# Performance work log

Hardware: AMD Instinct MI355X
Metric: run time of the kernel (lower is better)

## Reference

```python
import jax, jax.numpy as jnp
import numpy as np

EMA_A = 0.4      # exponential moving average decay used in Hash_ExpMovAverage
WIN = 9          # window_size
LN_EPS = 1e-3    # keras LayerNormalization default epsilon


def setup_inputs() -> dict:
    key = jax.random.key(0)
    ks = jax.random.split(key, 8)
    B, N, D, H = 8, 4096, 256, 8
    w = lambda k, shape: jax.random.normal(k, shape, jnp.float32) * 0.05
    return {
        "x": jax.random.normal(ks[0], (B, N, D), jnp.float32),
        "head_kernel": w(ks[1], (D, H, D)),
        "head_bias": w(ks[2], (H, D)),
        "down_kernel": w(ks[3], (H, D, D)),
        "down_bias": w(ks[4], (D,)),
        "value_kernel": w(ks[5], (D, D)),
        "value_bias": w(ks[6], (D,)),
        "ln_gamma": jnp.ones((D,), jnp.float32),
        "ln_beta": jnp.zeros((D,), jnp.float32),
    }


def reference(x, head_kernel, head_bias, down_kernel, down_bias,
              value_kernel, value_bias, ln_gamma, ln_beta):
    B, N, D = x.shape
    half = (WIN - 1) // 2

    # Up_Projection: [B,N,D] -> [B,N,H,D], relu
    q = jax.nn.relu(jnp.einsum('bnd,dhe->bnhe', x, head_kernel) + head_bias)

    # ---- Neighborhoods_Arrangement ----
    # Neighborhood_SimHash: sign codes from relu activations, summed over heads
    codes = 2.0 * jnp.minimum(jnp.ceil(q), 1.0) - 1.0        # [B,N,H,D]
    lsh = jnp.sum(codes, axis=-2)                            # [B,N,D]
    # Hash_ExpMovAverage: sort descending along D, add positional encoding, EMA dot
    pos = jnp.argsort(-lsh, axis=-1)                         # descending order
    lsh_sorted = jnp.take_along_axis(lsh, pos, axis=-1)
    pf = pos.astype(jnp.float32)
    freq = 10.0 ** (-(pf / jnp.float32(D)))                  # 1 / 10**powers
    pe = jnp.sin(freq) * (pf % 2) + jnp.cos(freq) * (1.0 - pf % 2)
    vals = lsh_sorted + pe / EMA_A
    c = EMA_A * (1.0 - EMA_A) ** jnp.arange(D, dtype=jnp.float32)
    simv = jnp.einsum('bnd,d->bn', vals, c)                  # [B,N]
    order = jnp.argsort(simv, axis=-1)                       # ascending
    q = jnp.take_along_axis(q, order[:, :, None, None], axis=1)  # reorder tokens

    # Down_Projection: [B,N,H,D] -> [B,N,D], relu
    q = jax.nn.relu(jnp.einsum('bnhd,hde->bne', q, down_kernel) + down_bias)

    # (matches tile-first / extract_patches / tile-last concat in the original)
    starts = jnp.clip(jnp.arange(N) - half, 0, N - WIN)      # [N]
    widx = starts[:, None] + jnp.arange(WIN)[None, :]
    keyw = q[:, widx]

    scale = jnp.sqrt(jnp.float32(D))
    scores = jax.nn.softmax(jnp.einsum('bnd,bnwd->bnw', q, keyw) / scale, axis=-1)
    value = jax.nn.relu(jnp.einsum('bnwd,de->bnwe', keyw, value_kernel) + value_bias)
    attn_out = jnp.einsum('bnwd,bnw->bnd', value, scores)

    # Residual with ORIGINAL (un-permuted) inputs + LayerNorm (keras default eps)
    y = attn_out + x
    mu = jnp.mean(y, axis=-1, keepdims=True)
    var = jnp.var(y, axis=-1, keepdims=True)
    return (y - mu) / jnp.sqrt(var + LN_EPS) * ln_gamma + ln_beta
```

## Files before the change

kernel.cpp:

```cpp
#include <hip/hip_runtime.h>

constexpr int Bc = 8, Nc = 4096;

using short8 = __attribute__((ext_vector_type(8))) short;
using f32x4  = __attribute__((ext_vector_type(4))) float;

static __device__ __forceinline__ unsigned short f2bf(float f) {
    unsigned u = __float_as_uint(f);
    u += 0x7fffu + ((u >> 16) & 1u);
    return (unsigned short)(u >> 16);
}
static __device__ __forceinline__ int swz(int r, int k) {
    return (r << 9) + ((k << 1) ^ ((r & 7) << 4));
}

__global__ __launch_bounds__(256)
void k0_wdt(const float* __restrict__ Wd, unsigned short* __restrict__ WdT)
{
    __shared__ float tile[64][65];
    const int h  = blockIdx.x >> 4;
    const int t  = blockIdx.x & 15;
    const int kb = (t >> 2) * 64, eb = (t & 3) * 64;
    const int tid = threadIdx.x;
    {
        const int krow = tid >> 2, ec = (tid & 3) * 16;
        const float* src = Wd + h * 65536 + (kb + krow) * 256 + eb + ec;
        #pragma unroll
        for (int i = 0; i < 4; ++i) {
            float4 v = *reinterpret_cast<const float4*>(src + i * 4);
            tile[krow][ec + i * 4 + 0] = v.x;
            tile[krow][ec + i * 4 + 1] = v.y;
            tile[krow][ec + i * 4 + 2] = v.z;
            tile[krow][ec + i * 4 + 3] = v.w;
        }
    }
    __syncthreads();
    {
        const int erow = tid >> 2, dc = (tid & 3) * 16;
        unsigned short o[16];
        #pragma unroll
        for (int i = 0; i < 16; ++i) o[i] = f2bf(tile[dc + i][erow]);
        unsigned short* dst = WdT + h * 65536 + (eb + erow) * 256 + kb + dc;
        *reinterpret_cast<short8*>(dst)     = *reinterpret_cast<short8*>(&o[0]);
        *reinterpret_cast<short8*>(dst + 8) = *reinterpret_cast<short8*>(&o[8]);
    }
}

__global__ __launch_bounds__(256)
void k0_wht(const float* __restrict__ Wh, unsigned short* __restrict__ WhH,
            float* __restrict__ WhT)
{
    __shared__ float tile[64][65];
    const int h  = blockIdx.x >> 4;
    const int t  = blockIdx.x & 15;
    const int kb = (t >> 2) * 64, eb = (t & 3) * 64;
    const int tid = threadIdx.x;
    {
        const int krow = tid >> 2, ec = (tid & 3) * 16;
        const float* src = Wh + (kb + krow) * 2048 + h * 256 + eb + ec;
        #pragma unroll
        for (int i = 0; i < 4; ++i) {
            float4 v = *reinterpret_cast<const float4*>(src + i * 4);
            tile[krow][ec + i * 4 + 0] = v.x;
            tile[krow][ec + i * 4 + 1] = v.y;
            tile[krow][ec + i * 4 + 2] = v.z;
            tile[krow][ec + i * 4 + 3] = v.w;
        }
    }
    __syncthreads();
    {
        const int erow = tid >> 2, dc = (tid & 3) * 16;
        unsigned short o[16];
        float of[16];
        #pragma unroll
        for (int i = 0; i < 16; ++i) {
            of[i] = tile[dc + i][erow];
            o[i] = f2bf(of[i]);
        }
        const long base = (long)h * 65536 + (eb + erow) * 256 + kb + dc;
        *reinterpret_cast<short8*>(WhH + base)     = *reinterpret_cast<short8*>(&o[0]);
        *reinterpret_cast<short8*>(WhH + base + 8) = *reinterpret_cast<short8*>(&o[8]);
        #pragma unroll
        for (int i = 0; i < 16; i += 4)
            *reinterpret_cast<float4*>(WhT + base + i) = *reinterpret_cast<const float4*>(&of[i]);
    }
}

__global__ __launch_bounds__(256)
void k0_wvt(const float* __restrict__ Wv, unsigned short* __restrict__ WvT)
{
    __shared__ float tile[64][65];
    const int t  = blockIdx.x;
    const int kb = (t >> 2) * 64, eb = (t & 3) * 64;
    const int tid = threadIdx.x;
    {
        const int krow = tid >> 2, ec = (tid & 3) * 16;
        const float* src = Wv + (kb + krow) * 256 + eb + ec;
        #pragma unroll
        for (int i = 0; i < 4; ++i) {
            float4 v = *reinterpret_cast<const float4*>(src + i * 4);
            tile[krow][ec + i * 4 + 0] = v.x;
            tile[krow][ec + i * 4 + 1] = v.y;
            tile[krow][ec + i * 4 + 2] = v.z;
            tile[krow][ec + i * 4 + 3] = v.w;
        }
    }
    __syncthreads();
    {
        const int erow = tid >> 2, dc = (tid & 3) * 16;
        unsigned short o[16];
        #pragma unroll
        for (int i = 0; i < 16; ++i) o[i] = f2bf(tile[dc + i][erow]);
        unsigned short* dst = WvT + (eb + erow) * 256 + kb + dc;
        *reinterpret_cast<short8*>(dst)     = *reinterpret_cast<short8*>(&o[0]);
        *reinterpret_cast<short8*>(dst + 8) = *reinterpret_cast<short8*>(&o[8]);
    }
}

#define XSH_OFF  0
#define QTB_OFF  16384
#define VALQ_OFF 35072
#define PE_OFF   67840
#define CF_OFF   68864
#define CNT_OFF  69888
#define FCN_OFF  71936
#define FLS_OFF  71952
#define FLS_CAP  1536
#define GUARD    0.012f

__global__ __launch_bounds__(256, 2)
void k1_head_down(const float* __restrict__ x,
                  const float* __restrict__ bh,
                  const float* __restrict__ WhT,
                  const unsigned short* __restrict__ WhH,
                  const unsigned short* __restrict__ WdT, const float* __restrict__ bd,
                  float* __restrict__ z, float* __restrict__ simv)
{
    __shared__ __align__(16) char SM[78336];

    const int tid = threadIdx.x;
    const long rowbase = (long)blockIdx.x * 32;
    const int wavei = tid >> 6, lane = tid & 63;
    const int mrow = lane & 15, kgrp = lane >> 4;
    const int ebase = wavei * 64 + mrow;
    const int kfo = kgrp * 8;

    short8 hB[4][4], dB[4][4];
    #pragma unroll
    for (int i = 0; i < 4; ++i)
        #pragma unroll
        for (int nf = 0; nf < 4; ++nf)
            hB[i][nf] = *reinterpret_cast<const short8*>(
                &WhH[(ebase + nf * 16) * 256 + i * 32 + kfo]);

    {
        const int d = tid;
        const float u = -((float)d * 0.00390625f);
        const float freq = (float)pow(10.0, (double)u);
        const float pe = (d & 1) ? (float)sin((double)freq)
                                 : (float)cos((double)freq);
        ((float*)(SM + PE_OFF))[d] = __fdiv_rn(pe, 0.4f);
        ((float*)(SM + CF_OFF))[d] = __fmul_rn(0.4f, (float)pow((double)0.6f, (double)d));
    }
    if (tid == 0) *((int*)(SM + FCN_OFF)) = 0;
    {
        const int r = tid >> 3, kc = (tid & 7) * 32;
        const float* src = x + (rowbase + r) * 256 + kc;
        unsigned short oh[32];
        #pragma unroll
        for (int i = 0; i < 32; i += 4) {
            float4 v = *reinterpret_cast<const float4*>(src + i);
            oh[i + 0] = f2bf(v.x); oh[i + 1] = f2bf(v.y);
            oh[i + 2] = f2bf(v.z); oh[i + 3] = f2bf(v.w);
        }
        #pragma unroll
        for (int i = 0; i < 32; i += 8)
            *reinterpret_cast<short8*>(SM + XSH_OFF + swz(r, kc + i)) =
                *reinterpret_cast<short8*>(&oh[i]);
    }

    unsigned lshp[4] = {0u, 0u, 0u, 0u};
    f32x4 dacc[2][4];
    #pragma unroll
    for (int mt = 0; mt < 2; ++mt)
        #pragma unroll
        for (int nf = 0; nf < 4; ++nf) dacc[mt][nf] = (f32x4){0.f, 0.f, 0.f, 0.f};

    __syncthreads();

    for (int h = 0; h < 8; ++h) {
        const unsigned short* whh = WhH + ((long)h << 16);
        const unsigned short* wdh = WdT + ((long)h << 16);
        float bias[4];
        #pragma unroll
        for (int nf = 0; nf < 4; ++nf) bias[nf] = bh[(h << 8) + ebase + nf * 16];

        f32x4 hacc[2][4];
        #pragma unroll
        for (int mt = 0; mt < 2; ++mt)
            #pragma unroll
            for (int nf = 0; nf < 4; ++nf) hacc[mt][nf] = (f32x4){0.f, 0.f, 0.f, 0.f};
        #pragma unroll
        for (int kt = 0; kt < 8; ++kt) {
            const int k0 = kt * 32 + kfo;
            short8 a0 = *reinterpret_cast<const short8*>(SM + XSH_OFF + swz(mrow, k0));
            short8 a1 = *reinterpret_cast<const short8*>(SM + XSH_OFF + swz(16 + mrow, k0));
            if (kt < 4) {
                #pragma unroll
                for (int nf = 0; nf < 4; ++nf)
                    dB[kt][nf] = *reinterpret_cast<const short8*>(
                        &wdh[(ebase + nf * 16) * 256 + kt * 32 + kfo]);
            }
            #pragma unroll
            for (int nf = 0; nf < 4; ++nf) {
                hacc[0][nf] = __builtin_amdgcn_mfma_f32_16x16x32_bf16(a0, hB[kt & 3][nf], hacc[0][nf], 0, 0, 0);
                hacc[1][nf] = __builtin_amdgcn_mfma_f32_16x16x32_bf16(a1, hB[kt & 3][nf], hacc[1][nf], 0, 0, 0);
            }
            if (kt < 4) {
                #pragma unroll
                for (int nf = 0; nf < 4; ++nf)
                    hB[kt][nf] = *reinterpret_cast<const short8*>(
                        &whh[(ebase + nf * 16) * 256 + (kt + 4) * 32 + kfo]);
            }
        }
        #pragma unroll
        for (int mt = 0; mt < 2; ++mt) {
            #pragma unroll
            for (int nf = 0; nf < 4; ++nf) {
                const int e = ebase + nf * 16;
                #pragma unroll
                for (int reg = 0; reg < 4; ++reg) {
                    const int r = mt * 16 + kgrp * 4 + reg;
                    const float pre = __fadd_rn(hacc[mt][nf][reg], bias[nf]);
                    const unsigned pos = (pre > 0.0f) ? 1u : 0u;
                    const int j = mt * 16 + nf * 4 + reg;
                    lshp[j >> 3] += pos << (4 * (j & 7));
                    if (fabsf(pre) < GUARD) {
                        int idx = atomicAdd((int*)(SM + FCN_OFF), 1);
                        if (idx < FLS_CAP)
                            ((int*)(SM + FLS_OFF))[idx] =
                                r | (e << 5) | (h << 13) | ((int)pos << 16);
                    }
                    *reinterpret_cast<unsigned short*>(SM + QTB_OFF + swz(r, e)) =
                        f2bf(fmaxf(pre, 0.0f));
                }
            }
        }
        __syncthreads();
        #pragma unroll
        for (int ks = 0; ks < 8; ++ks) {
            const int k0 = ks * 32 + kfo;
            short8 a0 = *reinterpret_cast<const short8*>(SM + QTB_OFF + swz(mrow, k0));
            short8 a1 = *reinterpret_cast<const short8*>(SM + QTB_OFF + swz(16 + mrow, k0));
            #pragma unroll
            for (int nf = 0; nf < 4; ++nf) {
                dacc[0][nf] = __builtin_amdgcn_mfma_f32_16x16x32_bf16(a0, dB[ks & 3][nf], dacc[0][nf], 0, 0, 0);
                dacc[1][nf] = __builtin_amdgcn_mfma_f32_16x16x32_bf16(a1, dB[ks & 3][nf], dacc[1][nf], 0, 0, 0);
            }
            if (ks < 4) {
                #pragma unroll
                for (int nf = 0; nf < 4; ++nf)
                    dB[ks][nf] = *reinterpret_cast<const short8*>(
                        &wdh[(ebase + nf * 16) * 256 + (ks + 4) * 32 + kfo]);
            } else if (h < 7) {
                #pragma unroll
                for (int nf = 0; nf < 4; ++nf)
                    hB[ks - 4][nf] = *reinterpret_cast<const short8*>(
                        &WhH[((long)(h + 1) << 16) + (ebase + nf * 16) * 256 + (ks - 4) * 32 + kfo]);
            }
        }
        __syncthreads();
    }
    #pragma unroll
    for (int mt = 0; mt < 2; ++mt) {
        #pragma unroll
        for (int nf = 0; nf < 4; ++nf) {
            const int e = ebase + nf * 16;
            const float b = bd[e];
            #pragma unroll
            for (int reg = 0; reg < 4; ++reg)
                z[(rowbase + mt * 16 + kgrp * 4 + reg) * 256 + e] =
                    fmaxf(dacc[mt][nf][reg] + b, 0.0f);
        }
    }
    {
        int* lshI = (int*)SM;
        #pragma unroll
        for (int mt = 0; mt < 2; ++mt)
            #pragma unroll
            for (int nf = 0; nf < 4; ++nf) {
                const int e = ebase + nf * 16;
                #pragma unroll
                for (int reg = 0; reg < 4; ++reg) {
                    const int r = mt * 16 + kgrp * 4 + reg;
                    const int j = mt * 16 + nf * 4 + reg;
                    const unsigned p = (lshp[j >> 3] >> (4 * (j & 7))) & 15u;
                    lshI[e * 34 + r] = 2 * (int)p - 8;
                }
            }
    }
    __syncthreads();
    {
        int* lshI = (int*)SM;
        int n = *((int*)(SM + FCN_OFF));
        n = n < FLS_CAP ? n : FLS_CAP;
        for (int i = tid; i < n; i += 256) {
            const int ent = ((int*)(SM + FLS_OFF))[i];
            const int r = ent & 31, e = (ent >> 5) & 255, hh2 = (ent >> 13) & 7;
            const int fs = ((ent >> 16) & 1) ? 1 : -1;
            const float* xr = x + (rowbase + r) * 256;
            const float* wrow = WhT + (((long)hh2 << 8) + e) * 256;
            float acc = 0.0f;
            for (int k = 0; k < 256; k += 4) {
                float4 xv = *reinterpret_cast<const float4*>(xr + k);
                float4 wv = *reinterpret_cast<const float4*>(wrow + k);
                acc = fmaf(xv.x, wv.x, acc);
                acc = fmaf(xv.y, wv.y, acc);
                acc = fmaf(xv.z, wv.z, acc);
                acc = fmaf(xv.w, wv.w, acc);
            }
            const float pre = __fadd_rn(acc, bh[hh2 * 256 + e]);
            const int es = (pre > 0.0f) ? 1 : -1;
            if (es != fs)
                atomicAdd(&lshI[e * 34 + r], es - fs);
        }
    }
    __syncthreads();
    if (tid < 32) {
        const int r = tid;
        const int* lshI = (const int*)SM;
        const float* pe_over = (const float*)(SM + PE_OFF);
        const float* c_f = (const float*)(SM + CF_OFF);
        int* cw = (int*)(SM + CNT_OFF) + r * 16;
        for (int i = 0; i < 9; ++i) cw[i] = 0;
        for (int d = 0; d < 256; ++d) {
            int vv = lshI[d * 34 + r];
            cw[(vv + 8) >> 1] += 1;
        }
        int run = 0;
        for (int bin = 8; bin >= 0; --bin) { int c0 = cw[bin]; cw[bin] = run; run += c0; }
        float* valq = (float*)(SM + VALQ_OFF + r * 1024);
        for (int d = 0; d < 256; ++d) {
            int vv = lshI[d * 34 + r];
            int bin = (vv + 8) >> 1;
            int j = cw[bin]++;
            valq[j] = __fadd_rn((float)vv, pe_over[d]);
        }
        float L0 = 0.f, L1 = 0.f, L2 = 0.f, L3 = 0.f,
              L4 = 0.f, L5 = 0.f, L6 = 0.f, L7 = 0.f;
        for (int i = 0; i < 256; i += 8) {
            L0 = fmaf(valq[i + 0], c_f[i + 0], L0);
            L1 = fmaf(valq[i + 1], c_f[i + 1], L1);
            L2 = fmaf(valq[i + 2], c_f[i + 2], L2);
            L3 = fmaf(valq[i + 3], c_f[i + 3], L3);
            L4 = fmaf(valq[i + 4], c_f[i + 4], L4);
            L5 = fmaf(valq[i + 5], c_f[i + 5], L5);
            L6 = fmaf(valq[i + 6], c_f[i + 6], L6);
            L7 = fmaf(valq[i + 7], c_f[i + 7], L7);
        }
        const float h0 = __fadd_rn(L0, L4);
        const float h1 = __fadd_rn(L1, L5);
        const float h2 = __fadd_rn(L2, L6);
        const float h3 = __fadd_rn(L3, L7);
        simv[rowbase + r] = __fadd_rn(__fadd_rn(h0, h2), __fadd_rn(h1, h3));
    }
}

__global__ __launch_bounds__(256)
void k2_rank(const float* __restrict__ simv, int* __restrict__ order)
{
    __shared__ float s_l[4096];
    const int b = blockIdx.x >> 4;
    const int chunk = blockIdx.x & 15;
    const float* S = simv + (long)b * 4096;
    for (int i = threadIdx.x; i < 4096; i += 256) s_l[i] = S[i];
    __syncthreads();
    const int n = chunk * 256 + threadIdx.x;
    const float key = s_l[n];
    int cnt = 0;
    for (int m = 0; m < 4096; ++m) {
        float sm = s_l[m];
        cnt += (sm < key) ? 1 : ((sm == key && m < n) ? 1 : 0);
    }
    order[(long)b * 4096 + cnt] = n;
}

__global__ __launch_bounds__(256, 3)
void k3_value(const float* __restrict__ z, const int* __restrict__ order,
              const unsigned short* __restrict__ WvT, const float* __restrict__ bv,
              float* __restrict__ v)
{
    __shared__ __align__(16) unsigned short ZB[32 * 256];
    __shared__ int ord[32];
    const int tid = threadIdx.x;
    const long rowbase = (long)blockIdx.x * 32;
    const long bbase = (rowbase >> 12) << 12;
    const int wavei = tid >> 6, lane = tid & 63;
    const int mrow = lane & 15, kgrp = lane >> 4;
    const int ebase = wavei * 64 + mrow;
    const int kfo = kgrp * 8;

    if (tid < 32) ord[tid] = order[rowbase + tid];

    short8 vB[4][4];
    #pragma unroll
    for (int i = 0; i < 4; ++i)
        #pragma unroll
        for (int nf = 0; nf < 4; ++nf)
            vB[i][nf] = *reinterpret_cast<const short8*>(
                &WvT[(ebase + nf * 16) * 256 + i * 32 + kfo]);

    __syncthreads();
    {
        const int r = tid >> 3, kc = (tid & 7) * 32;
        const float* src = z + (bbase + ord[r]) * 256 + kc;
        unsigned short oh[32];
        #pragma unroll
        for (int i = 0; i < 32; i += 4) {
            float4 vv = *reinterpret_cast<const float4*>(src + i);
            oh[i + 0] = f2bf(vv.x); oh[i + 1] = f2bf(vv.y);
            oh[i + 2] = f2bf(vv.z); oh[i + 3] = f2bf(vv.w);
        }
        #pragma unroll
        for (int i = 0; i < 32; i += 8)
            *reinterpret_cast<short8*>((char*)ZB + swz(r, kc + i)) =
                *reinterpret_cast<short8*>(&oh[i]);
    }
    __syncthreads();

    f32x4 acc[2][4];
    #pragma unroll
    for (int mt = 0; mt < 2; ++mt)
        #pragma unroll
        for (int nf = 0; nf < 4; ++nf) acc[mt][nf] = (f32x4){0.f, 0.f, 0.f, 0.f};
    #pragma unroll
    for (int kt = 0; kt < 8; ++kt) {
        const int k0 = kt * 32 + kfo;
        short8 a0 = *reinterpret_cast<const short8*>((char*)ZB + swz(mrow, k0));
        short8 a1 = *reinterpret_cast<const short8*>((char*)ZB + swz(16 + mrow, k0));
        #pragma unroll
        for (int nf = 0; nf < 4; ++nf) {
            acc[0][nf] = __builtin_amdgcn_mfma_f32_16x16x32_bf16(a0, vB[kt & 3][nf], acc[0][nf], 0, 0, 0);
            acc[1][nf] = __builtin_amdgcn_mfma_f32_16x16x32_bf16(a1, vB[kt & 3][nf], acc[1][nf], 0, 0, 0);
        }
        if (kt < 4) {
            #pragma unroll
            for (int nf = 0; nf < 4; ++nf)
                vB[kt][nf] = *reinterpret_cast<const short8*>(
                    &WvT[(ebase + nf * 16) * 256 + (kt + 4) * 32 + kfo]);
        }
    }
    #pragma unroll
    for (int mt = 0; mt < 2; ++mt) {
        #pragma unroll
        for (int nf = 0; nf < 4; ++nf) {
            const int e = ebase + nf * 16;
            const float b = bv[e];
            #pragma unroll
            for (int reg = 0; reg < 4; ++reg)
                v[(rowbase + mt * 16 + kgrp * 4 + reg) * 256 + e] =
                    fmaxf(acc[mt][nf][reg] + b, 0.0f);
        }
    }
}

__global__ __launch_bounds__(256)
void k4_attn_ln(const float* __restrict__ z, const float* __restrict__ v,
                const int* __restrict__ order, const float* __restrict__ x,
                const float* __restrict__ gamma, const float* __restrict__ beta,
                float* __restrict__ out)
{
    const int tid = threadIdx.x;
    const int wv = tid >> 6, lane = tid & 63;
    const long row = (long)blockIdx.x * 4 + wv;
    const int n = (int)(row & 4095);
    const long bbase = row - n;
    int start = n - 4;
    start = start < 0 ? 0 : start;
    start = start > (Nc - 9) ? (Nc - 9) : start;
    const int d0 = lane * 4;

    const int srcq = order[bbase + n];
    float4 q4 = *reinterpret_cast<const float4*>(&z[(bbase + srcq) * 256 + d0]);

    float t[9];
    #pragma unroll
    for (int w = 0; w < 9; ++w) {
        int srcm = order[bbase + start + w];
        float4 kv = *reinterpret_cast<const float4*>(&z[(bbase + srcm) * 256 + d0]);
        float p = q4.x * kv.x + q4.y * kv.y + q4.z * kv.z + q4.w * kv.w;
        #pragma unroll
        for (int off = 32; off > 0; off >>= 1) p += __shfl_xor(p, off);
        t[w] = p * 0.0625f;
    }
    float mx = t[0];
    #pragma unroll
    for (int w = 1; w < 9; ++w) mx = fmaxf(mx, t[w]);
    float pw[9], psum = 0.0f;
    #pragma unroll
    for (int w = 0; w < 9; ++w) { pw[w] = expf(t[w] - mx); psum += pw[w]; }
    const float pinv = 1.0f / psum;

    float4 a = make_float4(0.f, 0.f, 0.f, 0.f);
    #pragma unroll
    for (int w = 0; w < 9; ++w) {
        float4 vv = *reinterpret_cast<const float4*>(&v[(bbase + start + w) * 256 + d0]);
        float s = pw[w] * pinv;
        a.x = fmaf(vv.x, s, a.x);
        a.y = fmaf(vv.y, s, a.y);
        a.z = fmaf(vv.z, s, a.z);
        a.w = fmaf(vv.w, s, a.w);
    }
    float4 xv = *reinterpret_cast<const float4*>(&x[(bbase + n) * 256 + d0]);
    float4 y = make_float4(a.x + xv.x, a.y + xv.y, a.z + xv.z, a.w + xv.w);

    float s1 = y.x + y.y + y.z + y.w;
    float s2 = y.x * y.x + y.y * y.y + y.z * y.z + y.w * y.w;
    #pragma unroll
    for (int off = 32; off > 0; off >>= 1) {
        s1 += __shfl_xor(s1, off);
        s2 += __shfl_xor(s2, off);
    }
    const float mu = s1 * (1.0f / 256.0f);
    const float var = s2 * (1.0f / 256.0f) - mu * mu;
    const float istd = 1.0f / sqrtf(var + 0.001f);

    float4 g4 = *reinterpret_cast<const float4*>(&gamma[d0]);
    float4 b4 = *reinterpret_cast<const float4*>(&beta[d0]);
    float4 o;
    o.x = (y.x - mu) * istd * g4.x + b4.x;
    o.y = (y.y - mu) * istd * g4.y + b4.y;
    o.z = (y.z - mu) * istd * g4.z + b4.z;
    o.w = (y.w - mu) * istd * g4.w + b4.w;
    *reinterpret_cast<float4*>(&out[row * 256 + d0]) = o;
}

extern "C" void kernel_launch(void* const* d_in, const int* in_sizes, int n_in,
                              void* d_out, int out_size, void* d_ws, size_t ws_size,
                              hipStream_t stream)
{
    const float* x  = (const float*)d_in[0];
    const float* Wh = (const float*)d_in[1];
    const float* bh = (const float*)d_in[2];
    const float* Wd = (const float*)d_in[3];
    const float* bd = (const float*)d_in[4];
    const float* Wv = (const float*)d_in[5];
    const float* bv = (const float*)d_in[6];
    const float* g  = (const float*)d_in[7];
    const float* be = (const float*)d_in[8];
    float* out = (float*)d_out;

    char* ws = (char*)d_ws;
    float*          z     = (float*)ws;
    float*          v     = (float*)(ws + 33554432);
    float*          simv  = (float*)(ws + 67108864);
    int*            order = (int*)(ws + 67239936);
    unsigned short* WdT   = (unsigned short*)(ws + 67371008);
    unsigned short* WhH   = (unsigned short*)(ws + 68419584);
    float*          WhT   = (float*)(ws + 69468160);
    unsigned short* WvT   = (unsigned short*)(ws + 71565312);

    const int rows = Bc * Nc;
    k0_wdt<<<dim3(128), dim3(256), 0, stream>>>(Wd, WdT);
    k0_wht<<<dim3(128), dim3(256), 0, stream>>>(Wh, WhH, WhT);
    k0_wvt<<<dim3(16), dim3(256), 0, stream>>>(Wv, WvT);
    k1_head_down<<<dim3(rows / 32), dim3(256), 0, stream>>>(x, bh, WhT, WhH, WdT, bd, z, simv);
    k2_rank<<<dim3(Bc * 16), dim3(256), 0, stream>>>(simv, order);
    k3_value<<<dim3(rows / 32), dim3(256), 0, stream>>>(z, order, WvT, bv, v);
    k4_attn_ln<<<dim3(rows / 4), dim3(256), 0, stream>>>(z, v, order, x, g, be, out);
}
```

Baseline: 744.2 us.

## Shrink k1 shared memory and weight register buffers to raise occupancy

Compacts k1's LDS layout. The lsh counts become int8, the valq scratch reuses the front of shared memory, and the fallback list shrinks, so the block fits in under 50 KB and the launch bound rises from 2 to 3 blocks per CU. The 4-slot weight register ring in k1 and k3 becomes a 3-slot ring prefetched two k-steps ahead, which lowers VGPR pressure but leaves less latency slack per load. The lsh correction atomics are replaced by a bounded list that one thread applies serially, and x loads and z stores use nontemporal hints. Risks are overflow of the smaller caps (1024 and 96 entries) and more exposed global-load latency.

```diff
diff --git a/kernel.cpp b/kernel.cpp
--- a/kernel.cpp
+++ b/kernel.cpp
@@ -119,16 +119,19 @@
 
 #define XSH_OFF  0
 #define QTB_OFF  16384
-#define VALQ_OFF 35072
-#define PE_OFF   67840
-#define CF_OFF   68864
-#define CNT_OFF  69888
-#define FCN_OFF  71936
-#define FLS_OFF  71952
-#define FLS_CAP  1536
+#define LSH8_OFF 32768
+#define PE_OFF   40960
+#define CF_OFF   41984
+#define CNT_OFF  43008
+#define FCN_OFF  45056
+#define CCN_OFF  45060
+#define FLS_OFF  45064
+#define CLS_OFF  49160
+#define FLS_CAP  1024
+#define CLS_CAP  96
 #define GUARD    0.012f
 
-__global__ __launch_bounds__(256, 2)
+__global__ __launch_bounds__(256, 3)
 void k1_head_down(const float* __restrict__ x,
                   const float* __restrict__ bh,
                   const float* __restrict__ WhT,
@@ -136,7 +139,7 @@
                   const unsigned short* __restrict__ WdT, const float* __restrict__ bd,
                   float* __restrict__ z, float* __restrict__ simv)
 {
-    __shared__ __align__(16) char SM[78336];
+    __shared__ __align__(16) char SM[49600];
 
     const int tid = threadIdx.x;
     const long rowbase = (long)blockIdx.x * 32;
@@ -145,9 +148,9 @@
     const int ebase = wavei * 64 + mrow;
     const int kfo = kgrp * 8;
 
-    short8 hB[4][4], dB[4][4];
-    #pragma unroll
-    for (int i = 0; i < 4; ++i)
+    short8 hB[3][4], dB[3][4];
+    #pragma unroll
+    for (int i = 0; i < 2; ++i)
         #pragma unroll
         for (int nf = 0; nf < 4; ++nf)
             hB[i][nf] = *reinterpret_cast<const short8*>(
@@ -162,16 +165,16 @@
         ((float*)(SM + PE_OFF))[d] = __fdiv_rn(pe, 0.4f);
         ((float*)(SM + CF_OFF))[d] = __fmul_rn(0.4f, (float)pow((double)0.6f, (double)d));
     }
-    if (tid == 0) *((int*)(SM + FCN_OFF)) = 0;
+    if (tid == 0) { *((int*)(SM + FCN_OFF)) = 0; *((int*)(SM + CCN_OFF)) = 0; }
     {
         const int r = tid >> 3, kc = (tid & 7) * 32;
         const float* src = x + (rowbase + r) * 256 + kc;
         unsigned short oh[32];
         #pragma unroll
         for (int i = 0; i < 32; i += 4) {
-            float4 v = *reinterpret_cast<const float4*>(src + i);
-            oh[i + 0] = f2bf(v.x); oh[i + 1] = f2bf(v.y);
-            oh[i + 2] = f2bf(v.z); oh[i + 3] = f2bf(v.w);
+            f32x4 v = __builtin_nontemporal_load(reinterpret_cast<const f32x4*>(src + i));
+            oh[i + 0] = f2bf(v[0]); oh[i + 1] = f2bf(v[1]);
+            oh[i + 2] = f2bf(v[2]); oh[i + 3] = f2bf(v[3]);
         }
         #pragma unroll
         for (int i = 0; i < 32; i += 8)
@@ -205,24 +208,25 @@
             const int k0 = kt * 32 + kfo;
             short8 a0 = *reinterpret_cast<const short8*>(SM + XSH_OFF + swz(mrow, k0));
             short8 a1 = *reinterpret_cast<const short8*>(SM + XSH_OFF + swz(16 + mrow, k0));
-            if (kt < 4) {
+            if (kt < 6) {
                 #pragma unroll
                 for (int nf = 0; nf < 4; ++nf)
-                    dB[kt][nf] = *reinterpret_cast<const short8*>(
-                        &wdh[(ebase + nf * 16) * 256 + kt * 32 + kfo]);
+                    hB[(kt + 2) % 3][nf] = *reinterpret_cast<const short8*>(
+                        &whh[(ebase + nf * 16) * 256 + (kt + 2) * 32 + kfo]);
             }
             #pragma unroll
             for (int nf = 0; nf < 4; ++nf) {
-                hacc[0][nf] = __builtin_amdgcn_mfma_f32_16x16x32_bf16(a0, hB[kt & 3][nf], hacc[0][nf], 0, 0, 0);
-                hacc[1][nf] = __builtin_amdgcn_mfma_f32_16x16x32_bf16(a1, hB[kt & 3][nf], hacc[1][nf], 0, 0, 0);
-            }
-            if (kt < 4) {
-                #pragma unroll
-                for (int nf = 0; nf < 4; ++nf)
-                    hB[kt][nf] = *reinterpret_cast<const short8*>(
-                        &whh[(ebase + nf * 16) * 256 + (kt + 4) * 32 + kfo]);
-            }
-        }
+                hacc[0][nf] = __builtin_amdgcn_mfma_f32_16x16x32_bf16(a0, hB[kt % 3][nf], hacc[0][nf], 0, 0, 0);
+                hacc[1][nf] = __builtin_amdgcn_mfma_f32_16x16x32_bf16(a1, hB[kt % 3][nf], hacc[1][nf], 0, 0, 0);
+            }
+        }
+        #pragma unroll
+        for (int i = 0; i < 2; ++i)
+            #pragma unroll
+            for (int nf = 0; nf < 4; ++nf)
+                dB[i][nf] = *reinterpret_cast<const short8*>(
+                    &wdh[(ebase + nf * 16) * 256 + i * 32 + kfo]);
+
         #pragma unroll
         for (int mt = 0; mt < 2; ++mt) {
             #pragma unroll
@@ -252,21 +256,22 @@
             const int k0 = ks * 32 + kfo;
             short8 a0 = *reinterpret_cast<const short8*>(SM + QTB_OFF + swz(mrow, k0));
             short8 a1 = *reinterpret_cast<const short8*>(SM + QTB_OFF + swz(16 + mrow, k0));
-            #pragma unroll
-            for (int nf = 0; nf < 4; ++nf) {
-                dacc[0][nf] = __builtin_amdgcn_mfma_f32_16x16x32_bf16(a0, dB[ks & 3][nf], dacc[0][nf], 0, 0, 0);
-                dacc[1][nf] = __builtin_amdgcn_mfma_f32_16x16x32_bf16(a1, dB[ks & 3][nf], dacc[1][nf], 0, 0, 0);
-            }
-            if (ks < 4) {
+            if (ks < 6) {
                 #pragma unroll
                 for (int nf = 0; nf < 4; ++nf)
-                    dB[ks][nf] = *reinterpret_cast<const short8*>(
-                        &wdh[(ebase + nf * 16) * 256 + (ks + 4) * 32 + kfo]);
+                    dB[(ks + 2) % 3][nf] = *reinterpret_cast<const short8*>(
+                        &wdh[(ebase + nf * 16) * 256 + (ks + 2) * 32 + kfo]);
             } else if (h < 7) {
+                const int i = ks - 6;
                 #pragma unroll
                 for (int nf = 0; nf < 4; ++nf)
-                    hB[ks - 4][nf] = *reinterpret_cast<const short8*>(
-                        &WhH[((long)(h + 1) << 16) + (ebase + nf * 16) * 256 + (ks - 4) * 32 + kfo]);
+                    hB[i][nf] = *reinterpret_cast<const short8*>(
+                        &WhH[((long)(h + 1) << 16) + (ebase + nf * 16) * 256 + i * 32 + kfo]);
+            }
+            #pragma unroll
+            for (int nf = 0; nf < 4; ++nf) {
+                dacc[0][nf] = __builtin_amdgcn_mfma_f32_16x16x32_bf16(a0, dB[ks % 3][nf], dacc[0][nf], 0, 0, 0);
+                dacc[1][nf] = __builtin_amdgcn_mfma_f32_16x16x32_bf16(a1, dB[ks % 3][nf], dacc[1][nf], 0, 0, 0);
             }
         }
         __syncthreads();
@@ -279,12 +284,13 @@
             const float b = bd[e];
             #pragma unroll
             for (int reg = 0; reg < 4; ++reg)
-                z[(rowbase + mt * 16 + kgrp * 4 + reg) * 256 + e] =
-                    fmaxf(dacc[mt][nf][reg] + b, 0.0f);
-        }
-    }
-    {
-        int* lshI = (int*)SM;
+                __builtin_nontemporal_store(
+                    fmaxf(dacc[mt][nf][reg] + b, 0.0f),
+                    &z[(rowbase + mt * 16 + kgrp * 4 + reg) * 256 + e]);
+        }
+    }
+    {
+        signed char* lsh8 = (signed char*)(SM + LSH8_OFF);
         #pragma unroll
         for (int mt = 0; mt < 2; ++mt)
             #pragma unroll
@@ -295,13 +301,12 @@
                     const int r = mt * 16 + kgrp * 4 + reg;
                     const int j = mt * 16 + nf * 4 + reg;
                     const unsigned p = (lshp[j >> 3] >> (4 * (j & 7))) & 15u;
-                    lshI[e * 34 + r] = 2 * (int)p - 8;
+                    lsh8[e * 32 + r] = (signed char)(2 * (int)p - 8);
                 }
             }
     }
     __syncthreads();
     {
-        int* lshI = (int*)SM;
         int n = *((int*)(SM + FCN_OFF));
         n = n < FLS_CAP ? n : FLS_CAP;
         for (int i = tid; i < n; i += 256) {
@@ -321,27 +326,42 @@
             }
             const float pre = __fadd_rn(acc, bh[hh2 * 256 + e]);
             const int es = (pre > 0.0f) ? 1 : -1;
-            if (es != fs)
-                atomicAdd(&lshI[e * 34 + r], es - fs);
+            if (es != fs) {
+                int ci = atomicAdd((int*)(SM + CCN_OFF), 1);
+                if (ci < CLS_CAP)
+                    ((int*)(SM + CLS_OFF))[ci] = r | (e << 5) | ((es > 0 ? 1 : 0) << 13);
+            }
+        }
+    }
+    __syncthreads();
+    if (tid == 0) {
+        signed char* lsh8 = (signed char*)(SM + LSH8_OFF);
+        int cn = *((int*)(SM + CCN_OFF));
+        cn = cn < CLS_CAP ? cn : CLS_CAP;
+        for (int i = 0; i < cn; ++i) {
+            const int ent = ((int*)(SM + CLS_OFF))[i];
+            const int r = ent & 31, e = (ent >> 5) & 255;
+            const int d = ((ent >> 13) & 1) ? 2 : -2;
+            lsh8[e * 32 + r] = (signed char)(lsh8[e * 32 + r] + d);
         }
     }
     __syncthreads();
     if (tid < 32) {
         const int r = tid;
-        const int* lshI = (const int*)SM;
+        const signed char* lsh8 = (const signed char*)(SM + LSH8_OFF);
         const float* pe_over = (const float*)(SM + PE_OFF);
         const float* c_f = (const float*)(SM + CF_OFF);
         int* cw = (int*)(SM + CNT_OFF) + r * 16;
         for (int i = 0; i < 9; ++i) cw[i] = 0;
         for (int d = 0; d < 256; ++d) {
-            int vv = lshI[d * 34 + r];
+            int vv = (int)lsh8[d * 32 + r];
             cw[(vv + 8) >> 1] += 1;
         }
         int run = 0;
         for (int bin = 8; bin >= 0; --bin) { int c0 = cw[bin]; cw[bin] = run; run += c0; }
-        float* valq = (float*)(SM + VALQ_OFF + r * 1024);
+        float* valq = (float*)(SM + r * 1024);
         for (int d = 0; d < 256; ++d) {
-            int vv = lshI[d * 34 + r];
+            int vv = (int)lsh8[d * 32 + r];
             int bin = (vv + 8) >> 1;
             int j = cw[bin]++;
             valq[j] = __fadd_rn((float)vv, pe_over[d]);
@@ -402,9 +422,9 @@
 
     if (tid < 32) ord[tid] = order[rowbase + tid];
 
-    short8 vB[4][4];
-    #pragma unroll
-    for (int i = 0; i < 4; ++i)
+    short8 vB[3][4];
+    #pragma unroll
+    for (int i = 0; i < 2; ++i)
         #pragma unroll
         for (int nf = 0; nf < 4; ++nf)
             vB[i][nf] = *reinterpret_cast<const short8*>(
@@ -438,16 +458,16 @@
         const int k0 = kt * 32 + kfo;
         short8 a0 = *reinterpret_cast<const short8*>((char*)ZB + swz(mrow, k0));
         short8 a1 = *reinterpret_cast<const short8*>((char*)ZB + swz(16 + mrow, k0));
+        if (kt < 6) {
+            #pragma unroll
+            for (int nf = 0; nf < 4; ++nf)
+                vB[(kt + 2) % 3][nf] = *reinterpret_cast<const short8*>(
+                    &WvT[(ebase + nf * 16) * 256 + (kt + 2) * 32 + kfo]);
+        }
         #pragma unroll
         for (int nf = 0; nf < 4; ++nf) {
-            acc[0][nf] = __builtin_amdgcn_mfma_f32_16x16x32_bf16(a0, vB[kt & 3][nf], acc[0][nf], 0, 0, 0);
-            acc[1][nf] = __builtin_amdgcn_mfma_f32_16x16x32_bf16(a1, vB[kt & 3][nf], acc[1][nf], 0, 0, 0);
-        }
-        if (kt < 4) {
-            #pragma unroll
-            for (int nf = 0; nf < 4; ++nf)
-                vB[kt][nf] = *reinterpret_cast<const short8*>(
-                    &WvT[(ebase + nf * 16) * 256 + (kt + 4) * 32 + kfo]);
+            acc[0][nf] = __builtin_amdgcn_mfma_f32_16x16x32_bf16(a0, vB[kt % 3][nf], acc[0][nf], 0, 0, 0);
+            acc[1][nf] = __builtin_amdgcn_mfma_f32_16x16x32_bf16(a1, vB[kt % 3][nf], acc[1][nf], 0, 0, 0);
         }
     }
     #pragma unroll
```

Measured after the change: 834.9 us. 1.12x slower.
